# Performance work log

Measured on AMD Instinct MI355X. Metric: run time of the kernel, lower is better.

## Reference

```python
import jax, jax.numpy as jnp
import numpy as np

B, S, HID, ENC = 64, 1024, 1024, 2048
NEG = -1e10

def setup_inputs() -> dict:
    key = jax.random.key(0)
    k1, k2, k3, k4, k5 = jax.random.split(key, 5)
    decoder_hidden = jax.random.normal(k1, (B, HID), dtype=jnp.float32)
    encoder_outputs = jax.random.normal(k2, (B, S, ENC), dtype=jnp.float32)
    mask = jnp.ones((B, S), dtype=jnp.int32)
    # learned params (torch nn.Linear weight layout: [out, in]; no bias)
    Wq = jax.random.normal(k3, (HID, HID), dtype=jnp.float32) / np.sqrt(HID)
    Wk = jax.random.normal(k4, (HID, ENC), dtype=jnp.float32) / np.sqrt(ENC)
    v = jax.random.normal(k5, (HID,), dtype=jnp.float32) / np.sqrt(HID)
    return {"decoder_hidden": decoder_hidden, "encoder_outputs": encoder_outputs,
            "mask": mask, "Wq": Wq, "Wk": Wk, "v": v}

def reference(decoder_hidden, encoder_outputs, mask, Wq, Wk, v):
    # query: [B, 1, HID]
    query = (decoder_hidden @ Wq.T)[:, None, :]
    # keys: [B, S, HID]
    keys = jnp.einsum('bse,he->bsh', encoder_outputs, Wk)
    # energy: [B, S]  (v-projection of tanh(query + keys))
    energy = jnp.einsum('bsh,h->bs', jnp.tanh(query + keys), v)
    energy = jnp.where(mask == 0, jnp.float32(NEG), energy)
    attn_weights = jax.nn.softmax(energy, axis=1)
    # context: [B, ENC]
    context = jnp.einsum('bs,bse->be', attn_weights, encoder_outputs)
    return context, attn_weights
```

## Files before the change

kernel.cpp:

```cpp
#include <hip/hip_runtime.h>
#include <hip/hip_bf16.h>


#define B_   64
#define S_   1024
#define HID_ 1024
#define ENC_ 2048

typedef unsigned short u16;
typedef float  f32x4  __attribute__((ext_vector_type(4)));
typedef __bf16 bf16x8 __attribute__((ext_vector_type(8)));
typedef u16    u16x8  __attribute__((ext_vector_type(8)));

__device__ __forceinline__ u16 f2bf(float f) {
    unsigned u = __float_as_uint(f);
    u += 0x7FFFu + ((u >> 16) & 1u);
    return (u16)(u >> 16);
}
__device__ __forceinline__ float bf2f(u16 h) {
    return __uint_as_float(((unsigned)h) << 16);
}

__device__ __forceinline__ void gload16(const void* g, void* l) {
    __builtin_amdgcn_global_load_lds(
        (const __attribute__((address_space(1))) unsigned int*)g,
        (__attribute__((address_space(3))) unsigned int*)l,
        16, 0, 0);
}

__global__ __launch_bounds__(256) void cvt_kernel(const float* __restrict__ in,
                                                  u16* __restrict__ out, long n8) {
    long stride = (long)gridDim.x * blockDim.x;
    for (long i = (long)blockIdx.x * blockDim.x + threadIdx.x; i < n8; i += stride) {
        const float4* p = (const float4*)(in + (i << 3));
        float4 a = p[0], c = p[1];
        u16x8 o;
        o[0] = f2bf(a.x); o[1] = f2bf(a.y); o[2] = f2bf(a.z); o[3] = f2bf(a.w);
        o[4] = f2bf(c.x); o[5] = f2bf(c.y); o[6] = f2bf(c.z); o[7] = f2bf(c.w);
        *(u16x8*)(out + (i << 3)) = o;
    }
}

__global__ __launch_bounds__(256) void query_kernel(const float* __restrict__ dh,
                                                    const float* __restrict__ Wq,
                                                    float* __restrict__ q) {
    int b = blockIdx.y, eq = blockIdx.x, t = threadIdx.x;
    __shared__ float sdh[256];
    sdh[t] = dh[(b << 10) + (eq << 8) + t];
    __syncthreads();
    float s[4] = {0.f, 0.f, 0.f, 0.f};
    const float* wbase = Wq + (eq << 8);
    for (int e = 0; e < 256; e += 4) {
        float4 d = *(const float4*)(sdh + e);
        #pragma unroll
        for (int r = 0; r < 4; ++r) {
            int h = t + (r << 8);
            float4 wv = *(const float4*)(wbase + (size_t)h * HID_ + e);
            s[r] += wv.x * d.x + wv.y * d.y + wv.z * d.z + wv.w * d.w;
        }
    }
    #pragma unroll
    for (int r = 0; r < 4; ++r) atomicAdd(&q[(b << 10) + t + (r << 8)], s[r]);
}

__global__ __launch_bounds__(256) void keys_gemm(const u16* __restrict__ A,
                                                 const u16* __restrict__ Bw,
                                                 const float* __restrict__ q,
                                                 const float* __restrict__ v,
                                                 float* __restrict__ energy) {
    __shared__ u16 lds[16384];
    int bid = blockIdx.x;
    int swz = ((bid & 7) << 9) + (bid >> 3);
    int mt = swz >> 3, nt = swz & 7;
    int t = threadIdx.x;
    int w = t >> 6, l = t & 63;
    int lr = l >> 3, lc = l & 7;
    int srcsw = ((lc ^ lr) << 3);
    const u16* Abase = A + ((size_t)(mt << 7)) * ENC_;
    const u16* Bbase = Bw + ((size_t)(nt << 7)) * ENC_;
    char* ldsA = (char*)lds;
    char* ldsB = (char*)lds + 16384;
    int srow = (w << 5) + lr;
    int dstoff = (w << 12) + (l << 4);
    int lhi = l >> 4, llo = l & 15;
    int wm = w >> 1, wn = w & 1;
    int asw = (llo & 7) << 4;
    f32x4 acc[4][4] = {};

    for (int kt = 0; kt < ENC_; kt += 64) {
        #pragma unroll
        for (int p = 0; p < 4; ++p) {
            gload16(Abase + (size_t)(srow + (p << 3)) * ENC_ + kt + srcsw,
                    ldsA + dstoff + (p << 10));
            gload16(Bbase + (size_t)(srow + (p << 3)) * ENC_ + kt + srcsw,
                    ldsB + dstoff + (p << 10));
        }
        __syncthreads();
        #pragma unroll
        for (int kk = 0; kk < 64; kk += 32) {
            bf16x8 af[4], bf[4];
            int cb = ((kk << 1) + (lhi << 4)) ^ asw;
            #pragma unroll
            for (int i = 0; i < 4; ++i)
                af[i] = *(const bf16x8*)(ldsA + (((wm << 6) + (i << 4) + llo) << 7) + cb);
            #pragma unroll
            for (int j = 0; j < 4; ++j)
                bf[j] = *(const bf16x8*)(ldsB + (((wn << 6) + (j << 4) + llo) << 7) + cb);
            #pragma unroll
            for (int i = 0; i < 4; ++i)
                #pragma unroll
                for (int j = 0; j < 4; ++j)
                    acc[i][j] = __builtin_amdgcn_mfma_f32_16x16x32_bf16(
                        af[i], bf[j], acc[i][j], 0, 0, 0);
        }
        __syncthreads();
    }

    int b = mt >> 3;
    float qv[4], vv[4];
    #pragma unroll
    for (int j = 0; j < 4; ++j) {
        int h = (nt << 7) + (wn << 6) + (j << 4) + llo;
        qv[j] = q[(b << 10) + h];
        vv[j] = v[h];
    }
    #pragma unroll
    for (int i = 0; i < 4; ++i) {
        #pragma unroll
        for (int r = 0; r < 4; ++r) {
            float part = 0.f;
            #pragma unroll
            for (int j = 0; j < 4; ++j)
                part += tanhf(qv[j] + acc[i][j][r]) * vv[j];
            part += __shfl_down(part, 8);
            part += __shfl_down(part, 4);
            part += __shfl_down(part, 2);
            part += __shfl_down(part, 1);
            if (llo == 0) {
                int m = (mt << 7) + (wm << 6) + (i << 4) + (lhi << 2) + r;
                atomicAdd(&energy[m], part);
            }
        }
    }
}

__global__ __launch_bounds__(256) void softmax_kernel(const float* __restrict__ energy,
                                                      const int* __restrict__ mask,
                                                      float* __restrict__ attn) {
    int b = blockIdx.x, t = threadIdx.x;
    int w = t >> 6, l = t & 63;
    __shared__ float rmax[4], rsum[4];
    float4 e = *(const float4*)(energy + (b << 10) + (t << 2));
    int4 mk = *(const int4*)(mask + (b << 10) + (t << 2));
    if (mk.x == 0) e.x = -1e10f;
    if (mk.y == 0) e.y = -1e10f;
    if (mk.z == 0) e.z = -1e10f;
    if (mk.w == 0) e.w = -1e10f;
    float mx = fmaxf(fmaxf(e.x, e.y), fmaxf(e.z, e.w));
    for (int off = 32; off >= 1; off >>= 1) mx = fmaxf(mx, __shfl_xor(mx, off));
    if (l == 0) rmax[w] = mx;
    __syncthreads();
    mx = fmaxf(fmaxf(rmax[0], rmax[1]), fmaxf(rmax[2], rmax[3]));
    float4 ex;
    ex.x = expf(e.x - mx); ex.y = expf(e.y - mx);
    ex.z = expf(e.z - mx); ex.w = expf(e.w - mx);
    float sm = ex.x + ex.y + ex.z + ex.w;
    for (int off = 32; off >= 1; off >>= 1) sm += __shfl_xor(sm, off);
    if (l == 0) rsum[w] = sm;
    __syncthreads();
    sm = rsum[0] + rsum[1] + rsum[2] + rsum[3];
    float inv = 1.0f / sm;
    ex.x *= inv; ex.y *= inv; ex.z *= inv; ex.w *= inv;
    *(float4*)(attn + (b << 10) + (t << 2)) = ex;
}

__global__ __launch_bounds__(256) void context_kernel(const u16* __restrict__ enc_bf,
                                                      const float* __restrict__ attn,
                                                      float* __restrict__ ctx) {
    int b = blockIdx.y;
    int s0 = blockIdx.x << 7;
    int t = threadIdx.x;
    int e0 = t << 3;
    float acc[8] = {};
    const u16* base = enc_bf + ((size_t)((b << 10) + s0)) * ENC_ + e0;
    const float* wp = attn + (b << 10) + s0;
    for (int s = 0; s < 128; ++s) {
        float wgt = wp[s];
        u16x8 u = *(const u16x8*)(base + (size_t)s * ENC_);
        #pragma unroll
        for (int k = 0; k < 8; ++k) acc[k] += wgt * bf2f(u[k]);
    }
    float* cb = ctx + (b << 11) + e0;
    #pragma unroll
    for (int k = 0; k < 8; ++k) atomicAdd(&cb[k], acc[k]);
}

extern "C" void kernel_launch(void* const* d_in, const int* in_sizes, int n_in,
                              void* d_out, int out_size, void* d_ws, size_t ws_size,
                              hipStream_t stream) {
    const float* dh   = (const float*)d_in[0];
    const float* enc  = (const float*)d_in[1];
    const int*   mask = (const int*)d_in[2];
    const float* Wq   = (const float*)d_in[3];
    const float* Wk   = (const float*)d_in[4];
    const float* v    = (const float*)d_in[5];
    float* out  = (float*)d_out;
    float* ctx  = out;
    float* attn = out + B_ * ENC_;

    const size_t ENC_BF_BYTES = (size_t)B_ * S_ * ENC_ * 2;
    const size_t WK_BF_BYTES  = (size_t)HID_ * ENC_ * 2;
    const size_t Q_BYTES      = (size_t)B_ * HID_ * 4;
    const size_t E_BYTES      = (size_t)B_ * S_ * 4;
    if (ws_size < ENC_BF_BYTES + WK_BF_BYTES + Q_BYTES + E_BYTES) return;

    char* ws = (char*)d_ws;
    u16*   enc_bf = (u16*)ws;
    u16*   wk_bf  = (u16*)(ws + ENC_BF_BYTES);
    float* qbuf   = (float*)(ws + ENC_BF_BYTES + WK_BF_BYTES);
    float* energy = (float*)(ws + ENC_BF_BYTES + WK_BF_BYTES + Q_BYTES);

    hipMemsetAsync(qbuf, 0, Q_BYTES, stream);
    hipMemsetAsync(energy, 0, E_BYTES, stream);
    hipMemsetAsync(d_out, 0, (size_t)out_size * 4, stream);

    cvt_kernel<<<2048, 256, 0, stream>>>(enc, enc_bf, (long)((size_t)B_ * S_ * ENC_ / 8));
    cvt_kernel<<<128, 256, 0, stream>>>(Wk, wk_bf, (long)((size_t)HID_ * ENC_ / 8));
    query_kernel<<<dim3(4, B_), 256, 0, stream>>>(dh, Wq, qbuf);
    keys_gemm<<<4096, 256, 0, stream>>>(enc_bf, wk_bf, qbuf, v, energy);
    softmax_kernel<<<B_, 256, 0, stream>>>(energy, mask, attn);
    context_kernel<<<dim3(8, B_), 256, 0, stream>>>(enc_bf, attn, ctx);
}
```

Baseline: 1.308 ms.

## Rewrite keys GEMM as 256x256 double-buffered 8-wave pipeline; restructure query kernel

The keys GEMM moves from 128x128 tiles with 4 waves and a single LDS buffer to 256x256 tiles with 8 waves. It double-buffers 128 KB of LDS, interleaves global-to-LDS loads with MFMA phases under explicit barriers and vmcnt waits, and raises priority around the MFMA blocks. The goal is to hide load latency and cut global traffic per FLOP through larger reuse, at the cost of occupancy and fragile manual synchronisation. The query kernel is also rewritten to keep one Wq row per wave in registers and loop over the batch, which removes its atomics and the q memset.

```diff
diff --git a/kernel.cpp b/kernel.cpp
--- a/kernel.cpp
+++ b/kernel.cpp
@@ -27,6 +27,11 @@
         (__attribute__((address_space(3))) unsigned int*)l,
         16, 0, 0);
 }
+
+#define BAR() __builtin_amdgcn_s_barrier()
+#define LG0() do { asm volatile("s_waitcnt lgkmcnt(0)" ::: "memory"); \
+                   __builtin_amdgcn_sched_barrier(0); } while (0)
+#define VM4() asm volatile("s_waitcnt vmcnt(4)" ::: "memory")
 
 __global__ __launch_bounds__(256) void cvt_kernel(const float* __restrict__ in,
                                                   u16* __restrict__ out, long n8) {
@@ -44,88 +49,139 @@
 __global__ __launch_bounds__(256) void query_kernel(const float* __restrict__ dh,
                                                     const float* __restrict__ Wq,
                                                     float* __restrict__ q) {
-    int b = blockIdx.y, eq = blockIdx.x, t = threadIdx.x;
-    __shared__ float sdh[256];
-    sdh[t] = dh[(b << 10) + (eq << 8) + t];
-    __syncthreads();
-    float s[4] = {0.f, 0.f, 0.f, 0.f};
-    const float* wbase = Wq + (eq << 8);
-    for (int e = 0; e < 256; e += 4) {
-        float4 d = *(const float4*)(sdh + e);
-        #pragma unroll
-        for (int r = 0; r < 4; ++r) {
-            int h = t + (r << 8);
-            float4 wv = *(const float4*)(wbase + (size_t)h * HID_ + e);
-            s[r] += wv.x * d.x + wv.y * d.y + wv.z * d.z + wv.w * d.w;
+    int w = threadIdx.x >> 6, l = threadIdx.x & 63;
+    int h = (blockIdx.x << 2) + w;
+    float4 wv[4];
+    const float* wrow = Wq + (size_t)h * HID_;
+    #pragma unroll
+    for (int it = 0; it < 4; ++it) wv[it] = *(const float4*)(wrow + (it << 8) + (l << 2));
+    for (int b = 0; b < 64; ++b) {
+        const float* dr = dh + (b << 10);
+        float s = 0.f;
+        #pragma unroll
+        for (int it = 0; it < 4; ++it) {
+            float4 d = *(const float4*)(dr + (it << 8) + (l << 2));
+            s += wv[it].x * d.x + wv[it].y * d.y + wv[it].z * d.z + wv[it].w * d.w;
         }
-    }
-    #pragma unroll
-    for (int r = 0; r < 4; ++r) atomicAdd(&q[(b << 10) + t + (r << 8)], s[r]);
-}
-
-__global__ __launch_bounds__(256) void keys_gemm(const u16* __restrict__ A,
-                                                 const u16* __restrict__ Bw,
-                                                 const float* __restrict__ q,
-                                                 const float* __restrict__ v,
-                                                 float* __restrict__ energy) {
-    __shared__ u16 lds[16384];
+        #pragma unroll
+        for (int off = 32; off >= 1; off >>= 1) s += __shfl_xor(s, off);
+        if (l == 0) q[(b << 10) + h] = s;
+    }
+}
+
+__global__ __launch_bounds__(512, 2) void keys_gemm(const u16* __restrict__ A,
+                                                    const u16* __restrict__ Bw,
+                                                    const float* __restrict__ q,
+                                                    const float* __restrict__ v,
+                                                    float* __restrict__ energy) {
+    __shared__ char smem[131072];
     int bid = blockIdx.x;
-    int swz = ((bid & 7) << 9) + (bid >> 3);
-    int mt = swz >> 3, nt = swz & 7;
+    int wg = ((bid & 7) << 7) + (bid >> 3);
+    int mt = wg >> 2, nt = wg & 3;
     int t = threadIdx.x;
     int w = t >> 6, l = t & 63;
-    int lr = l >> 3, lc = l & 7;
-    int srcsw = ((lc ^ lr) << 3);
-    const u16* Abase = A + ((size_t)(mt << 7)) * ENC_;
-    const u16* Bbase = Bw + ((size_t)(nt << 7)) * ENC_;
-    char* ldsA = (char*)lds;
-    char* ldsB = (char*)lds + 16384;
-    int srow = (w << 5) + lr;
-    int dstoff = (w << 12) + (l << 4);
+    int wm = w >> 2, wn = w & 3;
     int lhi = l >> 4, llo = l & 15;
-    int wm = w >> 1, wn = w & 1;
-    int asw = (llo & 7) << 4;
-    f32x4 acc[4][4] = {};
-
-    for (int kt = 0; kt < ENC_; kt += 64) {
-        #pragma unroll
-        for (int p = 0; p < 4; ++p) {
-            gload16(Abase + (size_t)(srow + (p << 3)) * ENC_ + kt + srcsw,
-                    ldsA + dstoff + (p << 10));
-            gload16(Bbase + (size_t)(srow + (p << 3)) * ENC_ + kt + srcsw,
-                    ldsB + dstoff + (p << 10));
-        }
-        __syncthreads();
-        #pragma unroll
-        for (int kk = 0; kk < 64; kk += 32) {
-            bf16x8 af[4], bf[4];
-            int cb = ((kk << 1) + (lhi << 4)) ^ asw;
-            #pragma unroll
-            for (int i = 0; i < 4; ++i)
-                af[i] = *(const bf16x8*)(ldsA + (((wm << 6) + (i << 4) + llo) << 7) + cb);
-            #pragma unroll
-            for (int j = 0; j < 4; ++j)
-                bf[j] = *(const bf16x8*)(ldsB + (((wn << 6) + (j << 4) + llo) << 7) + cb);
-            #pragma unroll
-            for (int i = 0; i < 4; ++i)
+    const u16* Apan = A  + ((size_t)mt << 8) * ENC_;
+    const u16* Bpan = Bw + ((size_t)nt << 8) * ENC_;
+
+    int r0 = t >> 3, g0 = t & 7;
+    int r1 = (512 + t) >> 3, g1 = t & 7;
+    int c0 = (g0 ^ (r0 & 7)) << 3;
+    int c1 = (g1 ^ (r1 & 7)) << 3;
+
+    char* aHalf = smem + wm * 16384;
+    char* bHalf = smem + 32768 + (wn >> 1) * 16384;
+    int bRowO = (wn & 1) << 6;
+    int axor = (llo & 7) << 4;
+
+    f32x4 acc[8][4] = {};
+    bf16x8 a[4][2], b01[2][2], b23[2][2];
+
+    auto STAGE = [&](const u16* pan, int rowBase, int kt, int ldsOfs) {
+        gload16(pan + (size_t)(rowBase + r0) * ENC_ + kt + c0, smem + ldsOfs + (t << 4));
+        gload16(pan + (size_t)(rowBase + r1) * ENC_ + kt + c1, smem + ldsOfs + 8192 + (t << 4));
+    };
+    auto LDA = [&](int bufofs, int ibase) {
+        #pragma unroll
+        for (int ii = 0; ii < 4; ++ii)
+            #pragma unroll
+            for (int k = 0; k < 2; ++k)
+                a[ii][k] = *(const bf16x8*)(aHalf + bufofs +
+                    ((llo + ((ibase + ii) << 4)) << 7) + ((((k << 2) + lhi) << 4) ^ axor));
+    };
+    auto LDB = [&](bf16x8 (&bb)[2][2], int bufofs, int jbase) {
+        #pragma unroll
+        for (int j = 0; j < 2; ++j)
+            #pragma unroll
+            for (int k = 0; k < 2; ++k)
+                bb[j][k] = *(const bf16x8*)(bHalf + bufofs +
+                    ((bRowO + llo + ((jbase + j) << 4)) << 7) + ((((k << 2) + lhi) << 4) ^ axor));
+    };
+    auto MM = [&](bf16x8 (&bb)[2][2], int ibase, int jbase) {
+        __builtin_amdgcn_s_setprio(1);
+        #pragma unroll
+        for (int ii = 0; ii < 4; ++ii)
+            #pragma unroll
+            for (int j = 0; j < 2; ++j)
                 #pragma unroll
-                for (int j = 0; j < 4; ++j)
-                    acc[i][j] = __builtin_amdgcn_mfma_f32_16x16x32_bf16(
-                        af[i], bf[j], acc[i][j], 0, 0, 0);
-        }
-        __syncthreads();
-    }
-
-    int b = mt >> 3;
+                for (int k = 0; k < 2; ++k)
+                    acc[ibase + ii][jbase + j] = __builtin_amdgcn_mfma_f32_16x16x32_bf16(
+                        a[ii][k], bb[j][k], acc[ibase + ii][jbase + j], 0, 0, 0);
+        __builtin_amdgcn_s_setprio(0);
+    };
+
+    STAGE(Apan, 0,   0,  0);
+    STAGE(Apan, 128, 0,  16384);
+    STAGE(Bpan, 0,   0,  32768);
+    STAGE(Bpan, 128, 0,  49152);
+    STAGE(Bpan, 0,   64, 65536 + 32768);
+    STAGE(Bpan, 128, 64, 65536 + 49152);
+    VM4();
+    BAR();
+
+    #pragma unroll 1
+    for (int u = 0; u < 16; ++u) {
+        int ktA = u << 7, ktB = ktA + 64;
+        int ks2 = ktA + 128; if (ks2 >= ENC_) ks2 -= 128;
+        int ks3 = ktA + 192; if (ks3 >= ENC_) ks3 -= 128;
+
+        LDA(0, 0); LDB(b01, 0, 0);
+        STAGE(Apan, 0, ktB, 65536);
+        BAR(); LG0(); MM(b01, 0, 0); BAR();
+        LDB(b23, 0, 2);
+        STAGE(Apan, 128, ktB, 65536 + 16384);
+        BAR(); LG0(); MM(b23, 0, 2); BAR();
+        LDA(0, 4);
+        STAGE(Bpan, 0, ks2, 32768);
+        BAR(); LG0(); MM(b23, 4, 2); BAR();
+        STAGE(Bpan, 128, ks2, 49152);
+        VM4();
+        BAR(); LG0(); MM(b01, 4, 0); BAR();
+        LDA(65536, 0); LDB(b01, 65536, 0);
+        STAGE(Apan, 0, ks2, 0);
+        BAR(); LG0(); MM(b01, 0, 0); BAR();
+        LDB(b23, 65536, 2);
+        STAGE(Apan, 128, ks2, 16384);
+        BAR(); LG0(); MM(b23, 0, 2); BAR();
+        LDA(65536, 4);
+        STAGE(Bpan, 0, ks3, 65536 + 32768);
+        BAR(); LG0(); MM(b23, 4, 2); BAR();
+        STAGE(Bpan, 128, ks3, 65536 + 49152);
+        VM4();
+        BAR(); LG0(); MM(b01, 4, 0); BAR();
+    }
+
+    int b = mt >> 2;
     float qv[4], vv[4];
     #pragma unroll
     for (int j = 0; j < 4; ++j) {
-        int h = (nt << 7) + (wn << 6) + (j << 4) + llo;
+        int h = (nt << 8) + (wn << 6) + (j << 4) + llo;
         qv[j] = q[(b << 10) + h];
         vv[j] = v[h];
     }
     #pragma unroll
-    for (int i = 0; i < 4; ++i) {
+    for (int i = 0; i < 8; ++i) {
         #pragma unroll
         for (int r = 0; r < 4; ++r) {
             float part = 0.f;
@@ -137,7 +193,7 @@
             part += __shfl_down(part, 2);
             part += __shfl_down(part, 1);
             if (llo == 0) {
-                int m = (mt << 7) + (wm << 6) + (i << 4) + (lhi << 2) + r;
+                int m = (mt << 8) + (wm << 7) + (i << 4) + (lhi << 2) + r;
                 atomicAdd(&energy[m], part);
             }
         }
@@ -220,14 +276,13 @@
     float* qbuf   = (float*)(ws + ENC_BF_BYTES + WK_BF_BYTES);
     float* energy = (float*)(ws + ENC_BF_BYTES + WK_BF_BYTES + Q_BYTES);
 
-    hipMemsetAsync(qbuf, 0, Q_BYTES, stream);
     hipMemsetAsync(energy, 0, E_BYTES, stream);
     hipMemsetAsync(d_out, 0, (size_t)out_size * 4, stream);
 
     cvt_kernel<<<2048, 256, 0, stream>>>(enc, enc_bf, (long)((size_t)B_ * S_ * ENC_ / 8));
     cvt_kernel<<<128, 256, 0, stream>>>(Wk, wk_bf, (long)((size_t)HID_ * ENC_ / 8));
-    query_kernel<<<dim3(4, B_), 256, 0, stream>>>(dh, Wq, qbuf);
-    keys_gemm<<<4096, 256, 0, stream>>>(enc_bf, wk_bf, qbuf, v, energy);
+    query_kernel<<<256, 256, 0, stream>>>(dh, Wq, qbuf);
+    keys_gemm<<<1024, 512, 0, stream>>>(enc_bf, wk_bf, qbuf, v, energy);
     softmax_kernel<<<B_, 256, 0, stream>>>(energy, mask, attn);
     context_kernel<<<dim3(8, B_), 256, 0, stream>>>(enc_bf, attn, ctx);
 }
```

After: 1.125 ms. 1.16x faster.
